# Optimization experiments

Hardware: AMD Instinct MI355X
Metric: run time of the kernel (lower is better)

Reference implementation:

```python
import jax, jax.numpy as jnp
import numpy as np

N_NODES = 50000


def _scatter_softmax(alpha, row, n):
    # per-row-segment softmax over edges
    amax = jax.ops.segment_max(alpha, row, num_segments=n)
    amax = jnp.where(jnp.isfinite(amax), amax, 0.0)
    ex = jnp.exp(alpha - amax[row])
    den = jax.ops.segment_sum(ex, row, num_segments=n)
    return ex / den[row]


def setup_inputs() -> dict:
    key = jax.random.key(0)
    ks = jax.random.split(key, 10)
    N, E, H, NC, D = N_NODES, 500000, 128, 3, 3
    kv_in = H + NC * NC  # 137 (edges_in_d = 0)
    h = jax.random.normal(ks[0], (N, H), jnp.float32)
    coord = jax.random.normal(ks[1], (N, NC, D), jnp.float32)
    row = jax.random.randint(ks[2], (E,), 0, N, jnp.int32)
    col = jax.random.randint(ks[3], (E,), 0, N, jnp.int32)
    Wq = jax.random.normal(ks[4], (H, H), jnp.float32) / np.sqrt(H)
    bq = jnp.zeros((H,), jnp.float32)
    Wkv = jax.random.normal(ks[5], (kv_in, 2 * H), jnp.float32) / np.sqrt(kv_in)
    bkv = jnp.zeros((2 * H,), jnp.float32)
    Wc1 = jax.random.normal(ks[6], (H, 4 * H), jnp.float32) / np.sqrt(H)
    # torch.nn.init.xavier_uniform_(..., gain=0.001)
    Wc2 = jax.random.normal(ks[7], (4 * H, NC), jnp.float32) * 0.001
    return {"h": h, "coord": coord, "row": row, "col": col,
            "Wq": Wq, "bq": bq, "Wkv": Wkv, "bkv": bkv, "Wc1": Wc1, "Wc2": Wc2}


def reference(h, coord, row, col, Wq, bq, Wkv, bkv, Wc1, Wc2):
    N = h.shape[0]
    nc = coord.shape[1]
    # coord2radial (rm_F_norm=True: no normalization)
    coord_diff = coord[row] - coord[col]                      # [E, nc, d]
    radial = jnp.einsum('ecd,efd->ecf', coord_diff, coord_diff)  # [E, nc, nc]
    radial_flat = radial.reshape(radial.shape[0], nc * nc)
    # att_model: gather -> Q / KV linears -> interleaved k,v split
    q = h[row] @ Wq + bq                                      # [E, H]
    target_feat = jnp.concatenate([radial_flat, h[col]], axis=1)
    kv = target_feat @ Wkv + bkv                              # [E, 2H]
    k, v = kv[:, 0::2], kv[:, 1::2]
    alpha = jnp.sum(q * k, axis=1)                            # [E]
    alpha = _scatter_softmax(alpha, row, N)
    # node_model: scatter_sum aggregate (dropout is identity at eval)
    agg = jax.ops.segment_sum(alpha[:, None] * v, row, num_segments=N)
    h_out = h + agg
    # coord_model: coord_mlp(v) (MLPwoBias: linear -> SiLU -> linear, no biases)
    coord_v = alpha[:, None] * (jax.nn.silu(v @ Wc1) @ Wc2)   # [E, nc]
    trans = coord_diff * coord_v[:, :, None]                  # [E, nc, d]
    cagg = jax.ops.segment_sum(trans, row, num_segments=N)
    coord_out = coord + jnp.clip(cagg, -10.0, 10.0)
    return (h_out, coord_out, alpha)
```

## Files before the change

### kernel.cpp

```cpp
#include <hip/hip_runtime.h>

#define H 128
#define KV 256

typedef short bf16x8 __attribute__((ext_vector_type(8)));
typedef float f32x4 __attribute__((ext_vector_type(4)));
union FragU { uint4 u; bf16x8 s; };

#define LOG2E 1.44269504088896f
#define LN2   0.69314718055995f

__device__ __forceinline__ float bf2f(unsigned short u) {
  return __uint_as_float(((unsigned)u) << 16);
}
__device__ __forceinline__ unsigned short f2bf(float f) {
  unsigned b = __float_as_uint(f);
  b += 0x7FFFu + ((b >> 16) & 1u);
  return (unsigned short)(b >> 16);
}
__device__ __forceinline__ float fsilu(float x) {
  return x * __builtin_amdgcn_rcpf(1.f + __expf(-x));
}
__device__ __forceinline__ float fexp2(float x) {
  float r;
  asm("v_exp_f32 %0, %1" : "=v"(r) : "v"(x));
  return r;
}
__device__ __forceinline__ float fsilu2(float y) {
  return y * __builtin_amdgcn_rcpf(1.f + fexp2(-y));
}
__device__ __forceinline__ void rad6_from_cd(const float cd[9], float r6[6]) {
  r6[0] = cd[0]*cd[0] + cd[1]*cd[1] + cd[2]*cd[2];
  r6[1] = cd[3]*cd[3] + cd[4]*cd[4] + cd[5]*cd[5];
  r6[2] = cd[6]*cd[6] + cd[7]*cd[7] + cd[8]*cd[8];
  r6[3] = cd[0]*cd[3] + cd[1]*cd[4] + cd[2]*cd[5];
  r6[4] = cd[0]*cd[6] + cd[1]*cd[7] + cd[2]*cd[8];
  r6[5] = cd[3]*cd[6] + cd[4]*cd[7] + cd[5]*cd[8];
}
__constant__ int c_pa[6] = {0,4,8,1,2,5};
__constant__ int c_pb[6] = {0,0,0,3,6,7};

__global__ __launch_bounds__(256) void k_zero(float* __restrict__ p, int n) {
  int i = blockIdx.x * 256 + threadIdx.x;
  if (i < n) p[i] = 0.f;
}
__global__ __launch_bounds__(256) void k_sentinel(float* __restrict__ out, int n) {
  int i = blockIdx.x * 256 + threadIdx.x;
  if (i < n) out[i] = 1000.0f;
}

__global__ __launch_bounds__(256) void k_prep_w1(const float* __restrict__ Wc1,
                                                 uint4* __restrict__ w1f) {
  int t = blockIdx.x*256 + threadIdx.x;
  int g = t >> 6, lane = t & 63;
  int q = g >> 5, kk = (g >> 3) & 3, mt = g & 7;
  int o = q*128 + mt*16 + (lane & 15);
  int kbase = kk*32 + (lane >> 4)*8;
  unsigned s[8];
  #pragma unroll
  for (int j = 0; j < 8; ++j) s[j] = f2bf(Wc1[(kbase+j)*512 + o] * LOG2E);
  uint4 u;
  u.x = s[0] | (s[1]<<16); u.y = s[2] | (s[3]<<16);
  u.z = s[4] | (s[5]<<16); u.w = s[6] | (s[7]<<16);
  w1f[g*64 + lane] = u;
}

__global__ __launch_bounds__(256) void k_prep_wcat(
    const float* __restrict__ Wq, const float* __restrict__ Wkv,
    uint4* __restrict__ wcat_hi, uint4* __restrict__ wcat_lo)
{
  int t = blockIdx.x*256 + threadIdx.x;
  if (t >= 96*64) return;
  int g = t >> 6, lane = t & 63;
  int mt = g & 7, kk = (g >> 3) & 3, q = g >> 5;
  int oo = mt*16 + (lane & 15);
  int kbase = kk*32 + (lane >> 4)*8;
  unsigned shi[8], slo[8];
  #pragma unroll
  for (int j = 0; j < 8; ++j) {
    int k = kbase + j;
    float w;
    if (q == 0)      w = Wq[k*H + oo];
    else if (q == 1) w = Wkv[(9 + k)*KV + 2*oo];
    else             w = Wkv[(9 + k)*KV + 2*oo + 1];
    unsigned hi = f2bf(w);
    float lo = w - bf2f((unsigned short)hi);
    shi[j] = hi; slo[j] = f2bf(lo);
  }
  uint4 uh, ul;
  uh.x = shi[0]|(shi[1]<<16); uh.y = shi[2]|(shi[3]<<16);
  uh.z = shi[4]|(shi[5]<<16); uh.w = shi[6]|(shi[7]<<16);
  ul.x = slo[0]|(slo[1]<<16); ul.y = slo[2]|(slo[3]<<16);
  ul.z = slo[4]|(slo[5]<<16); ul.w = slo[6]|(slo[7]<<16);
  wcat_hi[g*64 + lane] = uh;
  wcat_lo[g*64 + lane] = ul;
}

__global__ __launch_bounds__(256) void k_prep_wr6(const float* __restrict__ Wkv,
                                                  const float* __restrict__ Wc1,
                                                  float* __restrict__ Wr6) {
  int idx = blockIdx.x*256 + threadIdx.x;
  if (idx >= 6*512) return;
  int d = idx >> 9, o = idx & 511;
  float s = 0.f;
  for (int k = 0; k < 128; ++k) {
    float w = Wkv[c_pa[d]*KV + 2*k + 1];
    if (d >= 3) w += Wkv[c_pb[d]*KV + 2*k + 1];
    s += w * Wc1[k*512 + o];
  }
  Wr6[d*512 + o] = s;
}

__global__ __launch_bounds__(256) void k_prep_ar6(
    const float* __restrict__ Wr6, const float* __restrict__ Wc2,
    uint4* __restrict__ ar6f, float* __restrict__ w2p)
{
  int t = threadIdx.x;
  for (int i = t; i < 512; i += 256) {
    int ch = i;
    unsigned b0 = (unsigned)f2bf(Wr6[0*512+ch]*LOG2E) | ((unsigned)f2bf(Wr6[1*512+ch]*LOG2E)<<16);
    unsigned b1 = (unsigned)f2bf(Wr6[2*512+ch]*LOG2E) | ((unsigned)f2bf(Wr6[3*512+ch]*LOG2E)<<16);
    unsigned b2 = (unsigned)f2bf(Wr6[4*512+ch]*LOG2E) | ((unsigned)f2bf(Wr6[5*512+ch]*LOG2E)<<16);
    ar6f[i] = make_uint4(b0, b1, b2, 0u);
  }
  for (int i = t; i < 1536; i += 256) {
    int i4 = i & 3, rest = i >> 2;
    int k = rest % 3, g = rest / 3;
    int ch = (g >> 2)*16 + (g & 3)*4 + i4;
    w2p[i] = Wc2[ch*3 + k] * LN2;
  }
}

__global__ __launch_bounds__(256) void k_hist2(const int* __restrict__ row,
                                               const int* __restrict__ col,
                                               int* __restrict__ cr,
                                               int* __restrict__ cc, int E) {
  int e = blockIdx.x*256 + threadIdx.x;
  if (e >= E) return;
  atomicAdd(&cr[row[e]], 1);
  atomicAdd(&cc[col[e]], 1);
}

__global__ __launch_bounds__(1024) void k_scan2(
    const int* __restrict__ cr, int* __restrict__ rstart, int* __restrict__ rcur,
    const int* __restrict__ cc, int* __restrict__ cstart, int* __restrict__ ccur,
    int n) {
  const int* counts = (blockIdx.x == 0) ? cr : cc;
  int* start = (blockIdx.x == 0) ? rstart : cstart;
  int* cursor = (blockIdx.x == 0) ? rcur : ccur;
  __shared__ int wsum[16];
  __shared__ int carry_s;
  const int tid = threadIdx.x, lane = tid & 63, wid = tid >> 6;
  if (tid == 0) carry_s = 0;
  __syncthreads();
  for (int base = 0; base < n; base += 1024) {
    int i = base + tid;
    int v = (i < n) ? counts[i] : 0;
    int s = v;
    #pragma unroll
    for (int off = 1; off < 64; off <<= 1) {
      int t = __shfl_up(s, off, 64);
      if (lane >= off) s += t;
    }
    if (lane == 63) wsum[wid] = s;
    __syncthreads();
    if (wid == 0 && lane < 16) {
      int w = wsum[lane];
      #pragma unroll
      for (int off = 1; off < 16; off <<= 1) {
        int t = __shfl_up(w, off, 16);
        if (lane >= off) w += t;
      }
      wsum[lane] = w;
    }
    __syncthreads();
    int wexcl = (wid == 0) ? 0 : wsum[wid-1];
    int excl = carry_s + wexcl + (s - v);
    if (i < n) { start[i] = excl; cursor[i] = excl; }
    __syncthreads();
    if (tid == 0) carry_s += wsum[15];
    __syncthreads();
  }
  if (threadIdx.x == 0) start[n] = carry_s;
}

__global__ __launch_bounds__(256) void k_scatter2(
    const int* __restrict__ row, const int* __restrict__ col,
    int* __restrict__ rcur, int* __restrict__ eidx,
    int* __restrict__ ccur, int* __restrict__ eidx2, int E) {
  int e = blockIdx.x*256 + threadIdx.x;
  if (e >= E) return;
  int pos = atomicAdd(&rcur[row[e]], 1);
  eidx[pos] = e;
  int pos2 = atomicAdd(&ccur[col[e]], 1);
  eidx2[pos2] = e;
}

__global__ __launch_bounds__(256) void k_node_mfma(
    const float* __restrict__ h, const uint4* __restrict__ wcat_hi,
    const uint4* __restrict__ wcat_lo, const float* __restrict__ bq,
    const float* __restrict__ bkv, float* __restrict__ qn,
    float* __restrict__ kn, unsigned short* __restrict__ vn, int N)
{
  __shared__ unsigned vhi[128*64];
  __shared__ unsigned vlo[128*64];
  const int tid = threadIdx.x;
  const int wid = tid >> 6, lane = tid & 63;
  const int quad = lane >> 4, colc = lane & 15;
  const int n0 = blockIdx.x * 128;
  for (int i = 0; i < 32; ++i) {
    int el = i*4 + wid;
    int c = n0 + el; if (c >= N) c = N - 1;
    float2 hv = *((const float2*)(h + (size_t)c*H + 2*lane));
    unsigned h0 = f2bf(hv.x), h1 = f2bf(hv.y);
    float l0 = hv.x - bf2f((unsigned short)h0);
    float l1 = hv.y - bf2f((unsigned short)h1);
    int sw = el*64 + (((lane>>2) ^ (el&15))<<2) + (lane&3);
    vhi[sw] = h0 | (h1<<16);
    vlo[sw] = (unsigned)f2bf(l0) | ((unsigned)f2bf(l1)<<16);
  }
  __syncthreads();
  const int ntbase = wid*32;
  for (int q = 0; q < 3; ++q) {
    f32x4 acc[8][2];
    #pragma unroll
    for (int mt = 0; mt < 8; ++mt)
      #pragma unroll
      for (int nt = 0; nt < 2; ++nt) acc[mt][nt] = (f32x4){0.f,0.f,0.f,0.f};
    #pragma unroll
    for (int kk = 0; kk < 4; ++kk) {
      FragU bhi[2], blo[2];
      #pragma unroll
      for (int nt = 0; nt < 2; ++nt) {
        int rrow = ntbase + nt*16 + colc;
        int ad = rrow*64 + (((kk*4 + quad) ^ (rrow&15))<<2);
        bhi[nt].u = *((const uint4*)&vhi[ad]);
        blo[nt].u = *((const uint4*)&vlo[ad]);
      }
      #pragma unroll
      for (int mt = 0; mt < 8; ++mt) {
        FragU ahi, alo;
        int gidx = (((q*4+kk)*8+mt)<<6) + lane;
        ahi.u = wcat_hi[gidx];
        alo.u = wcat_lo[gidx];
        #pragma unroll
        for (int nt = 0; nt < 2; ++nt) {
          acc[mt][nt] = __builtin_amdgcn_mfma_f32_16x16x32_bf16(
              ahi.s, bhi[nt].s, acc[mt][nt], 0, 0, 0);
          acc[mt][nt] = __builtin_amdgcn_mfma_f32_16x16x32_bf16(
              ahi.s, blo[nt].s, acc[mt][nt], 0, 0, 0);
          acc[mt][nt] = __builtin_amdgcn_mfma_f32_16x16x32_bf16(
              alo.s, bhi[nt].s, acc[mt][nt], 0, 0, 0);
        }
      }
    }
    #pragma unroll
    for (int mt = 0; mt < 8; ++mt)
      #pragma unroll
      for (int nt = 0; nt < 2; ++nt) {
        int node = n0 + ntbase + nt*16 + colc;
        if (node >= N) continue;
        int chq = mt*16 + quad*4;
        if (q == 0) {
          float4 b = *((const float4*)(bq + chq));
          float4 o;
          o.x = acc[mt][nt][0] + b.x; o.y = acc[mt][nt][1] + b.y;
          o.z = acc[mt][nt][2] + b.z; o.w = acc[mt][nt][3] + b.w;
          *((float4*)(qn + (size_t)node*H + chq)) = o;
        } else if (q == 1) {
          float4 o;
          o.x = acc[mt][nt][0] + bkv[2*(chq+0)];
          o.y = acc[mt][nt][1] + bkv[2*(chq+1)];
          o.z = acc[mt][nt][2] + bkv[2*(chq+2)];
          o.w = acc[mt][nt][3] + bkv[2*(chq+3)];
          *((float4*)(kn + (size_t)node*H + chq)) = o;
        } else {
          unsigned s0 = f2bf(acc[mt][nt][0] + bkv[2*(chq+0)+1]);
          unsigned s1 = f2bf(acc[mt][nt][1] + bkv[2*(chq+1)+1]);
          unsigned s2 = f2bf(acc[mt][nt][2] + bkv[2*(chq+2)+1]);
          unsigned s3 = f2bf(acc[mt][nt][3] + bkv[2*(chq+3)+1]);
          *((uint2*)(vn + (size_t)node*H + chq)) =
              make_uint2(s0 | (s1<<16), s2 | (s3<<16));
        }
      }
  }
}

__global__ __launch_bounds__(256) void k_qw(
    const float* __restrict__ qn, const float* __restrict__ Wkv,
    float* __restrict__ qwn, int N)
{
  __shared__ float wke6[6*128];
  const int tid = threadIdx.x;
  for (int idx = tid; idx < 6*128; idx += 256) {
    int d = idx >> 7, j = idx & 127;
    float we = Wkv[c_pa[d]*KV + 2*j];
    if (d >= 3) we += Wkv[c_pb[d]*KV + 2*j];
    wke6[idx] = we;
  }
  __syncthreads();
  const int wid = tid >> 6, lane = tid & 63;
  const int n = blockIdx.x*4 + wid;
  if (n >= N) return;
  float q0 = qn[(size_t)n*H + lane];
  float q1 = qn[(size_t)n*H + 64 + lane];
  #pragma unroll
  for (int d = 0; d < 6; ++d) {
    float p = q0*wke6[d*128 + lane] + q1*wke6[d*128 + 64 + lane];
    #pragma unroll
    for (int m = 32; m > 0; m >>= 1) p += __shfl_xor(p, m, 64);
    if (lane == 0) qwn[(size_t)n*6 + d] = p;
  }
}

__global__ __launch_bounds__(256) void k_edge_alpha(
    const float* __restrict__ coord, const int* __restrict__ row,
    const int* __restrict__ col, const int* __restrict__ eidx,
    const float* __restrict__ qn, const float* __restrict__ kn,
    const float* __restrict__ qwn, float* __restrict__ aout, int E)
{
  int j = blockIdx.x*256 + threadIdx.x;
  if (j >= E) return;
  int e = eidx[j];
  int r = row[e], c = col[e];
  const float4* qp = (const float4*)(qn + (size_t)r*H);
  const float4* kp = (const float4*)(kn + (size_t)c*H);
  float d0 = 0.f, d1 = 0.f, d2 = 0.f, d3 = 0.f;
  #pragma unroll 8
  for (int i = 0; i < 32; ++i) {
    float4 qv = qp[i], kv = kp[i];
    d0 += qv.x*kv.x; d1 += qv.y*kv.y;
    d2 += qv.z*kv.z; d3 += qv.w*kv.w;
  }
  float cd[9], r6[6];
  #pragma unroll
  for (int i = 0; i < 9; ++i)
    cd[i] = coord[(size_t)r*9 + i] - coord[(size_t)c*9 + i];
  rad6_from_cd(cd, r6);
  float ar = (d0 + d1) + (d2 + d3);
  #pragma unroll
  for (int d = 0; d < 6; ++d) ar += r6[d]*qwn[(size_t)r*6 + d];
  aout[e] = ar;
}

__global__ __launch_bounds__(256) void k_row_soft(
    const float* __restrict__ h, const float* __restrict__ coord,
    const int* __restrict__ col, const float* __restrict__ Wkv,
    const int* __restrict__ row_start, const int* __restrict__ eidx,
    const unsigned* __restrict__ vnu, float* __restrict__ aout,
    float* __restrict__ hout, int N)
{
  __shared__ float wvo6[6*128];
  __shared__ float ws[4][64];
  __shared__ int   cs[4][64];
  const int tid = threadIdx.x;
  for (int idx = tid; idx < 6*128; idx += 256) {
    int d = idx >> 7, jj = idx & 127;
    float wo = Wkv[c_pa[d]*KV + 2*jj + 1];
    if (d >= 3) wo += Wkv[c_pb[d]*KV + 2*jj + 1];
    wvo6[idx] = wo;
  }
  __syncthreads();
  const int wid = tid >> 6, lane = tid & 63;
  const int r = blockIdx.x*4 + wid;
  if (r >= N) return;
  const int js = row_start[r], je = row_start[r+1];
  const int deg = je - js;
  float crd[9];
  #pragma unroll
  for (int i = 0; i < 9; ++i) crd[i] = coord[(size_t)r*9 + i];

  float t6s[6];
  float mn, invl;
  const bool big = (deg > 64);
  if (!big) {
    int e = 0, c = 0;
    float ar = -1e30f;
    float r6[6] = {0.f,0.f,0.f,0.f,0.f,0.f};
    if (lane < deg) {
      e = eidx[js + lane];
      ar = aout[e];
      c = col[e];
      float cd[9];
      #pragma unroll
      for (int i = 0; i < 9; ++i) cd[i] = crd[i] - coord[(size_t)c*9 + i];
      rad6_from_cd(cd, r6);
    }
    float mx = ar;
    #pragma unroll
    for (int m = 32; m > 0; m >>= 1) mx = fmaxf(mx, __shfl_xor(mx, m, 64));
    mn = mx;
    float w = (lane < deg) ? __expf(ar - mn) : 0.f;
    float lw = w;
    #pragma unroll
    for (int m = 32; m > 0; m >>= 1) lw += __shfl_xor(lw, m, 64);
    invl = (deg > 0) ? 1.f/lw : 0.f;
    #pragma unroll
    for (int d = 0; d < 6; ++d) {
      float v = w*r6[d];
      #pragma unroll
      for (int m = 32; m > 0; m >>= 1) v += __shfl_xor(v, m, 64);
      t6s[d] = v;
    }
    ws[wid][lane] = w;
    cs[wid][lane] = c;
    if (lane < deg) aout[e] = w*invl;
  } else {
    float mx = -1e30f;
    for (int j2 = js + lane; j2 < je; j2 += 64)
      mx = fmaxf(mx, aout[eidx[j2]]);
    #pragma unroll
    for (int m = 32; m > 0; m >>= 1) mx = fmaxf(mx, __shfl_xor(mx, m, 64));
    mn = mx;
    float lp = 0.f;
    float t6p[6] = {0.f,0.f,0.f,0.f,0.f,0.f};
    for (int j2 = js + lane; j2 < je; j2 += 64) {
      int e = eidx[j2];
      float ar = aout[e];
      float w = __expf(ar - mn);
      lp += w;
      int c = col[e];
      float cd[9], r6[6];
      #pragma unroll
      for (int i = 0; i < 9; ++i) cd[i] = crd[i] - coord[(size_t)c*9 + i];
      rad6_from_cd(cd, r6);
      #pragma unroll
      for (int d = 0; d < 6; ++d) t6p[d] += w*r6[d];
    }
    #pragma unroll
    for (int m = 32; m > 0; m >>= 1) lp += __shfl_xor(lp, m, 64);
    invl = (deg > 0) ? 1.f/lp : 0.f;
    #pragma unroll
    for (int d = 0; d < 6; ++d) {
      float v = t6p[d];
      #pragma unroll
      for (int m = 32; m > 0; m >>= 1) v += __shfl_xor(v, m, 64);
      t6s[d] = v;
    }
  }
  float acc0 = 0.f, acc1 = 0.f;
  if (!big) {
    #pragma unroll 4
    for (int t = 0; t < deg; ++t) {
      float w = ws[wid][t];
      int c = cs[wid][t];
      unsigned v = vnu[(size_t)c*64 + lane];
      acc0 += w*__uint_as_float(v << 16);
      acc1 += w*__uint_as_float(v & 0xffff0000u);
    }
  } else {
    for (int t = js; t < je; ++t) {
      int e = eidx[t];
      float ar = aout[e];
      float w = __expf(ar - mn);
      int c = col[e];
      unsigned v = vnu[(size_t)c*64 + lane];
      acc0 += w*__uint_as_float(v << 16);
      acc1 += w*__uint_as_float(v & 0xffff0000u);
    }
    for (int j2 = js + lane; j2 < je; j2 += 64) {
      int e = eidx[j2];
      aout[e] = __expf(aout[e] - mn)*invl;
    }
  }
  float o0 = acc0, o1 = acc1;
  #pragma unroll
  for (int d = 0; d < 6; ++d) {
    o0 += t6s[d]*wvo6[d*128 + 2*lane];
    o1 += t6s[d]*wvo6[d*128 + 2*lane + 1];
  }
  hout[(size_t)r*H + 2*lane]     = h[(size_t)r*H + 2*lane]     + o0*invl;
  hout[(size_t)r*H + 2*lane + 1] = h[(size_t)r*H + 2*lane + 1] + o1*invl;
}

__global__ __launch_bounds__(256) void k_node_hn(
    const unsigned* __restrict__ vnu, const uint4* __restrict__ w1f,
    unsigned short* __restrict__ hn, int N)
{
  __shared__ unsigned vt[128*64];
  __shared__ unsigned short hno[128*128];
  const int tid = threadIdx.x;
  const int wid = tid >> 6, lane = tid & 63;
  const int quad = lane >> 4, colc = lane & 15;
  const int n0 = blockIdx.x * 128;
  for (int i = 0; i < 32; ++i) {
    int el = i*4 + wid;
    int c = n0 + el; if (c >= N) c = N - 1;
    unsigned pk = vnu[(size_t)c*64 + lane];
    vt[el*64 + (((lane>>2) ^ (el&15))<<2) + (lane&3)] = pk;
  }
  __syncthreads();
  const int ntbase = wid*32;
  for (int q = 0; q < 4; ++q) {
    f32x4 acc[8][2];
    #pragma unroll
    for (int mt = 0; mt < 8; ++mt)
      #pragma unroll
      for (int nt = 0; nt < 2; ++nt) acc[mt][nt] = (f32x4){0.f,0.f,0.f,0.f};
    #pragma unroll
    for (int kk = 0; kk < 4; ++kk) {
      FragU bfr[2];
      #pragma unroll
      for (int nt = 0; nt < 2; ++nt) {
        int rrow = ntbase + nt*16 + colc;
        int chunk = kk*4 + quad;
        bfr[nt].u = *((const uint4*)&vt[rrow*64 + ((chunk ^ (rrow&15))<<2)]);
      }
      #pragma unroll
      for (int mt = 0; mt < 8; ++mt) {
        FragU afr;
        afr.u = w1f[(((q*4+kk)*8+mt)<<6) + lane];
        #pragma unroll
        for (int nt = 0; nt < 2; ++nt)
          acc[mt][nt] = __builtin_amdgcn_mfma_f32_16x16x32_bf16(
              afr.s, bfr[nt].s, acc[mt][nt], 0, 0, 0);
      }
    }
    #pragma unroll
    for (int mt = 0; mt < 8; ++mt)
      #pragma unroll
      for (int nt = 0; nt < 2; ++nt) {
        int node = ntbase + nt*16 + colc;
        int o = mt*16 + quad*4;
        unsigned lo = (unsigned)f2bf(acc[mt][nt][0]) | ((unsigned)f2bf(acc[mt][nt][1]) << 16);
        unsigned hi = (unsigned)f2bf(acc[mt][nt][2]) | ((unsigned)f2bf(acc[mt][nt][3]) << 16);
        *((uint2*)&hno[node*128 + o]) = make_uint2(lo, hi);
      }
    __syncthreads();
    const uint4* hns = (const uint4*)hno;
    #pragma unroll
    for (int it = 0; it < 8; ++it) {
      int u = it*256 + tid;
      int node = u >> 4, within = u & 15;
      int gn = n0 + node;
      if (gn < N) ((uint4*)hn)[(size_t)gn*64 + q*16 + within] = hns[node*16 + within];
    }
    __syncthreads();
  }
}

__global__ __launch_bounds__(512) void k_edge_mlp3(
    const float* __restrict__ coord, const int* __restrict__ row,
    const int* __restrict__ col, const uint4* __restrict__ ar6f,
    const float* __restrict__ w2p, const unsigned short* __restrict__ hn,
    const int* __restrict__ eidx2, float* __restrict__ mlpout, int E)
{
  __shared__ uint4 a8[512];
  __shared__ float4 w2s[384];
  const int tid = threadIdx.x;
  {
    const uint4* s4 = (const uint4*)w2p;
    for (int i = tid; i < 512; i += 512) a8[i] = ar6f[i];
    if (tid < 384) w2s[tid] = ((const float4*)s4)[tid];
  }
  __syncthreads();
  const int wid = tid >> 6, lane = tid & 63;
  const int l15 = lane & 15, quad = lane >> 4;
  const bool q0 = (quad == 0);

  int gw = blockIdx.x*8 + wid;
  int nw = gridDim.x*8;
  int ntile = (E + 63) >> 6;
  for (int t = gw; t < ntile; t += nw) {
    int j = t*64 + lane;
    int jc = (j < E) ? j : (E - 1);
    int e = eidx2[jc];
    int c = col[e];
    int r = row[e];
    float cd[9], r6[6];
    #pragma unroll
    for (int i = 0; i < 9; ++i)
      cd[i] = coord[(size_t)r*9 + i] - coord[(size_t)c*9 + i];
    rad6_from_cd(cd, r6);
    unsigned pw0 = (unsigned)f2bf(r6[0]) | ((unsigned)f2bf(r6[1]) << 16);
    unsigned pw1 = (unsigned)f2bf(r6[2]) | ((unsigned)f2bf(r6[3]) << 16);
    unsigned pw2 = (unsigned)f2bf(r6[4]) | ((unsigned)f2bf(r6[5]) << 16);
    FragU bfr[4];
    const unsigned short* hb[4];
    #pragma unroll
    for (int f = 0; f < 4; ++f) {
      int src = f*16 + l15;
      unsigned w0 = __shfl(pw0, src, 64);
      unsigned w1 = __shfl(pw1, src, 64);
      unsigned w2_ = __shfl(pw2, src, 64);
      bfr[f].u = make_uint4(q0 ? w0 : 0u, q0 ? w1 : 0u, q0 ? w2_ : 0u, 0u);
      int nb = __shfl(c, src, 64);
      hb[f] = hn + (size_t)nb*512 + quad*4;
    }
    float cv[4][3];
    #pragma unroll
    for (int f = 0; f < 4; ++f) { cv[f][0]=0.f; cv[f][1]=0.f; cv[f][2]=0.f; }

    #pragma unroll 2
    for (int m = 0; m < 32; ++m) {
      uint4 av = a8[m*16 + l15];
      FragU afr;
      afr.u = make_uint4(q0 ? av.x : 0u, q0 ? av.y : 0u, q0 ? av.z : 0u, 0u);
      float4 wk0 = w2s[(m*4 + quad)*3 + 0];
      float4 wk1 = w2s[(m*4 + quad)*3 + 1];
      float4 wk2 = w2s[(m*4 + quad)*3 + 2];
      #pragma unroll
      for (int f = 0; f < 4; ++f) {
        uint2 hv = *((const uint2*)(hb[f] + m*16));
        f32x4 cin;
        cin[0] = __uint_as_float(hv.x << 16);
        cin[1] = __uint_as_float(hv.x & 0xffff0000u);
        cin[2] = __uint_as_float(hv.y << 16);
        cin[3] = __uint_as_float(hv.y & 0xffff0000u);
        f32x4 d = __builtin_amdgcn_mfma_f32_16x16x32_bf16(
            afr.s, bfr[f].s, cin, 0, 0, 0);
        float s0 = fsilu2(d[0]);
        float s1 = fsilu2(d[1]);
        float s2 = fsilu2(d[2]);
        float s3 = fsilu2(d[3]);
        cv[f][0] += s0*wk0.x + s1*wk0.y + s2*wk0.z + s3*wk0.w;
        cv[f][1] += s0*wk1.x + s1*wk1.y + s2*wk1.z + s3*wk1.w;
        cv[f][2] += s0*wk2.x + s1*wk2.y + s2*wk2.z + s3*wk2.w;
      }
    }
    #pragma unroll
    for (int f = 0; f < 4; ++f)
      #pragma unroll
      for (int k = 0; k < 3; ++k) {
        float v = cv[f][k];
        v += __shfl_xor(v, 16, 64);
        v += __shfl_xor(v, 32, 64);
        cv[f][k] = v;
      }
    #pragma unroll
    for (int f = 0; f < 4; ++f) {
      int src = f*16 + l15;
      int eb = __shfl(e, src, 64);
      int jb = t*64 + src;
      if (q0 && jb < E) {
        float* mp = &mlpout[(size_t)eb*3];
        mp[0] = cv[f][0]; mp[1] = cv[f][1]; mp[2] = cv[f][2];
      }
    }
  }
}

__global__ __launch_bounds__(256) void k_coord(
    const float* __restrict__ coord, const int* __restrict__ col,
    const int* __restrict__ row_start, const int* __restrict__ eidx,
    const float* __restrict__ aout, const float* __restrict__ mlpout,
    float* __restrict__ cout, int N)
{
  const int tid = threadIdx.x;
  const int wid = tid >> 6, lane = tid & 63;
  const int r = blockIdx.x*4 + wid;
  if (r >= N) return;
  const int js = row_start[r], je = row_start[r+1];
  float cr[9];
  #pragma unroll
  for (int i = 0; i < 9; ++i) cr[i] = coord[(size_t)r*9 + i];
  float cg[9] = {0.f,0.f,0.f,0.f,0.f,0.f,0.f,0.f,0.f};
  for (int j = js + lane; j < je; j += 64) {
    int e = eidx[j];
    float a = aout[e];
    int c = col[e];
    float cd[9];
    #pragma unroll
    for (int i = 0; i < 9; ++i) cd[i] = cr[i] - coord[(size_t)c*9 + i];
    float p0 = a*mlpout[(size_t)e*3+0];
    float p1 = a*mlpout[(size_t)e*3+1];
    float p2 = a*mlpout[(size_t)e*3+2];
    #pragma unroll
    for (int d = 0; d < 3; ++d) {
      cg[0+d] += p0*cd[0+d];
      cg[3+d] += p1*cd[3+d];
      cg[6+d] += p2*cd[6+d];
    }
  }
  #pragma unroll
  for (int i = 0; i < 9; ++i)
    #pragma unroll
    for (int m = 32; m > 0; m >>= 1) cg[i] += __shfl_xor(cg[i], m, 64);
  if (lane == 0) {
    #pragma unroll
    for (int i = 0; i < 9; ++i) {
      float x = fminf(10.f, fmaxf(-10.f, cg[i]));
      cout[(size_t)r*9 + i] = cr[i] + x;
    }
  }
}

extern "C" void kernel_launch(void* const* d_in, const int* in_sizes, int n_in,
                              void* d_out, int out_size, void* d_ws, size_t ws_size,
                              hipStream_t stream)
{
  const float* h     = (const float*)d_in[0];
  const float* coord = (const float*)d_in[1];
  const int* row = (const int*)d_in[2];
  const int* col = (const int*)d_in[3];
  const float* Wq  = (const float*)d_in[4];
  const float* bq  = (const float*)d_in[5];
  const float* Wkv = (const float*)d_in[6];
  const float* bkv = (const float*)d_in[7];
  const float* Wc1 = (const float*)d_in[8];
  const float* Wc2 = (const float*)d_in[9];
  const int N = in_sizes[0] / H;
  const int E = in_sizes[2];
  float* out = (float*)d_out;

  char* p = (char*)d_ws;
  float* qn = (float*)p;
  float* kn = (float*)(p + (size_t)N*H*4);
  unsigned short* hn = (unsigned short*)p;
  p += (size_t)N*H*8;
  unsigned short* vn = (unsigned short*)p;  p += (size_t)N*H*2;
  float* mlpout = (float*)p;                p += (size_t)E*3*4;
  int* counts_r = (int*)p;                  p += (size_t)N*4;
  int* counts_c = (int*)p;                  p += (size_t)N*4;
  int* row_start = (int*)p;                 p += (size_t)(N+1)*4;
  int* cursor_r = (int*)p;                  p += (size_t)N*4;
  int* cstart = (int*)p;                    p += (size_t)(N+1)*4;
  int* cursor_c = (int*)p;                  p += (size_t)N*4;
  int* eidx = (int*)p;                      p += (size_t)E*4;
  int* eidx2 = (int*)p;                     p += (size_t)E*4;
  uint4* w1f = (uint4*)((((size_t)p) + 15) & ~(size_t)15);
  float* Wr6 = (float*)((char*)w1f + 8192*16);
  uint4* ar6f = (uint4*)((char*)Wr6 + 6*512*4);
  float* w2p  = (float*)((char*)ar6f + 512*16);
  float* qwn  = (float*)((char*)w2p + 1536*4);
  uint4* wcat_hi = (uint4*)((char*)qwn + (size_t)N*6*4);
  uint4* wcat_lo = (uint4*)((char*)wcat_hi + 6144*16);
  const size_t need = (size_t)((char*)wcat_lo + 6144*16 - (char*)d_ws);

  if (ws_size < need) {
    k_sentinel<<<(out_size + 255)/256, 256, 0, stream>>>(out, out_size);
    return;
  }

  float* hout = out;
  float* cout = out + (size_t)N*H;
  float* aout = cout + (size_t)N*9;

  k_zero<<<(2*N + 255)/256, 256, 0, stream>>>((float*)counts_r, 2*N);
  k_prep_w1<<<32, 256, 0, stream>>>(Wc1, w1f);
  k_prep_wcat<<<24, 256, 0, stream>>>(Wq, Wkv, wcat_hi, wcat_lo);
  k_prep_wr6<<<12, 256, 0, stream>>>(Wkv, Wc1, Wr6);
  k_prep_ar6<<<1, 256, 0, stream>>>(Wr6, Wc2, ar6f, w2p);
  k_hist2<<<(E + 255)/256, 256, 0, stream>>>(row, col, counts_r, counts_c, E);
  k_node_mfma<<<(N + 127)/128, 256, 0, stream>>>(h, wcat_hi, wcat_lo, bq, bkv,
                                                 qn, kn, vn, N);
  k_qw<<<(N + 3)/4, 256, 0, stream>>>(qn, Wkv, qwn, N);
  k_scan2<<<2, 1024, 0, stream>>>(counts_r, row_start, cursor_r,
                                  counts_c, cstart, cursor_c, N);
  k_scatter2<<<(E + 255)/256, 256, 0, stream>>>(row, col, cursor_r, eidx,
                                                cursor_c, eidx2, E);
  k_edge_alpha<<<(E + 255)/256, 256, 0, stream>>>(coord, row, col, eidx,
                                                  qn, kn, qwn, aout, E);
  k_row_soft<<<(N + 3)/4, 256, 0, stream>>>(h, coord, col, Wkv, row_start, eidx,
                                            (const unsigned*)vn, aout, hout, N);
  k_node_hn<<<(N + 127)/128, 256, 0, stream>>>((const unsigned*)vn, w1f, hn, N);
  k_edge_mlp3<<<512, 512, 0, stream>>>(coord, row, col, ar6f, w2p,
                                       hn, eidx2, mlpout, E);
  k_coord<<<(N + 3)/4, 256, 0, stream>>>(coord, col, row_start, eidx, aout,
                                         mlpout, cout, N);
}
```

Baseline: 679.1 us.

## Fuse coordinate aggregation into edge MLP kernel via atomic scatter-add

The edge MLP kernel now multiplies its per-edge coord MLP output by alpha and the coordinate differences, then adds the result directly into a per-node accumulation buffer with float atomics. This replaces the separate per-row gather kernel and the per-edge mlpout round trip through memory. A small elementwise kernel then applies the clip and adds the original coordinates. In exchange it issues nine scattered atomics per edge, because edges are ordered by column and rows are therefore random. It also adds a zeroing launch, 18 KB of shared memory per block, and a non-deterministic summation order.

Result: slower. 826.3 us (+21.7%).

```diff
diff --git a/kernel.cpp b/kernel.cpp
--- a/kernel.cpp
+++ b/kernel.cpp
@@ -543,10 +543,12 @@
     const float* __restrict__ coord, const int* __restrict__ row,
     const int* __restrict__ col, const uint4* __restrict__ ar6f,
     const float* __restrict__ w2p, const unsigned short* __restrict__ hn,
-    const int* __restrict__ eidx2, float* __restrict__ mlpout, int E)
+    const int* __restrict__ eidx2, const float* __restrict__ aout,
+    float* __restrict__ cagg, int E)
 {
   __shared__ uint4 a8[512];
   __shared__ float4 w2s[384];
+  __shared__ float cds[512][9];
   const int tid = threadIdx.x;
   {
     const uint4* s4 = (const uint4*)w2p;
@@ -567,11 +569,14 @@
     int e = eidx2[jc];
     int c = col[e];
     int r = row[e];
+    float a = aout[e];
     float cd[9], r6[6];
     #pragma unroll
     for (int i = 0; i < 9; ++i)
       cd[i] = coord[(size_t)r*9 + i] - coord[(size_t)c*9 + i];
     rad6_from_cd(cd, r6);
+    #pragma unroll
+    for (int i = 0; i < 9; ++i) cds[tid][i] = cd[i];
     unsigned pw0 = (unsigned)f2bf(r6[0]) | ((unsigned)f2bf(r6[1]) << 16);
     unsigned pw1 = (unsigned)f2bf(r6[2]) | ((unsigned)f2bf(r6[3]) << 16);
     unsigned pw2 = (unsigned)f2bf(r6[4]) | ((unsigned)f2bf(r6[5]) << 16);
@@ -627,61 +632,29 @@
         v += __shfl_xor(v, 32, 64);
         cv[f][k] = v;
       }
-    #pragma unroll
-    for (int f = 0; f < 4; ++f) {
-      int src = f*16 + l15;
-      int eb = __shfl(e, src, 64);
-      int jb = t*64 + src;
-      if (q0 && jb < E) {
-        float* mp = &mlpout[(size_t)eb*3];
-        mp[0] = cv[f][0]; mp[1] = cv[f][1]; mp[2] = cv[f][2];
-      }
-    }
-  }
-}
-
-__global__ __launch_bounds__(256) void k_coord(
-    const float* __restrict__ coord, const int* __restrict__ col,
-    const int* __restrict__ row_start, const int* __restrict__ eidx,
-    const float* __restrict__ aout, const float* __restrict__ mlpout,
-    float* __restrict__ cout, int N)
-{
-  const int tid = threadIdx.x;
-  const int wid = tid >> 6, lane = tid & 63;
-  const int r = blockIdx.x*4 + wid;
-  if (r >= N) return;
-  const int js = row_start[r], je = row_start[r+1];
-  float cr[9];
-  #pragma unroll
-  for (int i = 0; i < 9; ++i) cr[i] = coord[(size_t)r*9 + i];
-  float cg[9] = {0.f,0.f,0.f,0.f,0.f,0.f,0.f,0.f,0.f};
-  for (int j = js + lane; j < je; j += 64) {
-    int e = eidx[j];
-    float a = aout[e];
-    int c = col[e];
-    float cd[9];
-    #pragma unroll
-    for (int i = 0; i < 9; ++i) cd[i] = cr[i] - coord[(size_t)c*9 + i];
-    float p0 = a*mlpout[(size_t)e*3+0];
-    float p1 = a*mlpout[(size_t)e*3+1];
-    float p2 = a*mlpout[(size_t)e*3+2];
-    #pragma unroll
-    for (int d = 0; d < 3; ++d) {
-      cg[0+d] += p0*cd[0+d];
-      cg[3+d] += p1*cd[3+d];
-      cg[6+d] += p2*cd[6+d];
-    }
-  }
-  #pragma unroll
-  for (int i = 0; i < 9; ++i)
-    #pragma unroll
-    for (int m = 32; m > 0; m >>= 1) cg[i] += __shfl_xor(cg[i], m, 64);
-  if (lane == 0) {
-    #pragma unroll
-    for (int i = 0; i < 9; ++i) {
-      float x = fminf(10.f, fmaxf(-10.f, cg[i]));
-      cout[(size_t)r*9 + i] = cr[i] + x;
-    }
+    if (j < E) {
+      float p0 = a*cv[quad][0];
+      float p1 = a*cv[quad][1];
+      float p2 = a*cv[quad][2];
+      float* cg = &cagg[(size_t)r*9];
+      #pragma unroll
+      for (int dd = 0; dd < 3; ++dd) {
+        atomicAdd(&cg[0+dd], p0*cds[tid][0+dd]);
+        atomicAdd(&cg[3+dd], p1*cds[tid][3+dd]);
+        atomicAdd(&cg[6+dd], p2*cds[tid][6+dd]);
+      }
+    }
+  }
+}
+
+__global__ __launch_bounds__(256) void k_coord_fin(
+    const float* __restrict__ coord, const float* __restrict__ cagg,
+    float* __restrict__ cout, int n9)
+{
+  int i = blockIdx.x*256 + threadIdx.x;
+  if (i < n9) {
+    float x = fminf(10.f, fmaxf(-10.f, cagg[i]));
+    cout[i] = coord[i] + x;
   }
 }
 
@@ -709,7 +682,7 @@
   unsigned short* hn = (unsigned short*)p;
   p += (size_t)N*H*8;
   unsigned short* vn = (unsigned short*)p;  p += (size_t)N*H*2;
-  float* mlpout = (float*)p;                p += (size_t)E*3*4;
+  float* cagg = (float*)p;                  p += (size_t)E*3*4;
   int* counts_r = (int*)p;                  p += (size_t)N*4;
   int* counts_c = (int*)p;                  p += (size_t)N*4;
   int* row_start = (int*)p;                 p += (size_t)(N+1)*4;
@@ -737,6 +710,7 @@
   float* aout = cout + (size_t)N*9;
 
   k_zero<<<(2*N + 255)/256, 256, 0, stream>>>((float*)counts_r, 2*N);
+  k_zero<<<(9*N + 255)/256, 256, 0, stream>>>(cagg, 9*N);
   k_prep_w1<<<32, 256, 0, stream>>>(Wc1, w1f);
   k_prep_wcat<<<24, 256, 0, stream>>>(Wq, Wkv, wcat_hi, wcat_lo);
   k_prep_wr6<<<12, 256, 0, stream>>>(Wkv, Wc1, Wr6);
@@ -755,7 +729,6 @@
                                             (const unsigned*)vn, aout, hout, N);
   k_node_hn<<<(N + 127)/128, 256, 0, stream>>>((const unsigned*)vn, w1f, hn, N);
   k_edge_mlp3<<<512, 512, 0, stream>>>(coord, row, col, ar6f, w2p,
-                                       hn, eidx2, mlpout, E);
-  k_coord<<<(N + 3)/4, 256, 0, stream>>>(coord, col, row_start, eidx, aout,
-                                         mlpout, cout, N);
-}
+                                       hn, eidx2, aout, cagg, E);
+  k_coord_fin<<<(9*N + 255)/256, 256, 0, stream>>>(coord, cagg, cout, 9*N);
+}
```
